# Optimization experiments

Measured on AMD Instinct MI355X. Metric: run time of the kernel, lower is better.

The kernel has to match this reference:

```python
import jax, jax.numpy as jnp
import numpy as np

N = 10000       # num_nodes
E = 160000      # num_edges
F = 128         # num_features
R = 20          # num_rbf_features
L = 3           # num_message_passing_layers
CUT = 3.0       # cutoff_dist
NA = 119        # num_unique_atoms + 1


def _safe_norm(x, axis=-1):
    sq = jnp.sum(x * x, axis=axis)
    return jnp.where(sq > 0, jnp.sqrt(jnp.where(sq > 0, sq, 1.0)), 0.0)


def setup_inputs() -> dict:
    key = jax.random.key(0)
    ks = jax.random.split(key, 20)
    s = 0.05  # weight init scale
    z = jax.random.randint(ks[0], (N,), 1, NA)
    pos = jax.random.uniform(ks[1], (N, 3), dtype=jnp.float32) * 4.0
    idx_i = jax.random.randint(ks[2], (E,), 0, N)
    off = jax.random.randint(ks[3], (E,), 1, N)
    idx_j = (idx_i + off) % N  # no self loops (radius_graph loop=False)
    emb = (jax.random.normal(ks[4], (NA, F), jnp.float32) * s).at[0].set(0.0)
    return {
        'z': z, 'pos': pos, 'idx_i': idx_i, 'idx_j': idx_j, 'emb': emb,
        'msg_w1': jax.random.normal(ks[5], (L, F, F), jnp.float32) * s,
        'msg_b1': jnp.zeros((L, F), jnp.float32),
        'msg_w2': jax.random.normal(ks[6], (L, F, 3 * F), jnp.float32) * s,
        'msg_b2': jnp.zeros((L, 3 * F), jnp.float32),
        'rbf_w': jax.random.normal(ks[7], (L, R, 3 * F), jnp.float32) * s,
        'rbf_b': jnp.zeros((L, 3 * F), jnp.float32),
        'upd_U': jax.random.normal(ks[8], (L, F, F), jnp.float32) * s,
        'upd_V': jax.random.normal(ks[9], (L, F, F), jnp.float32) * s,
        'upd_w1': jax.random.normal(ks[10], (L, 2 * F, F), jnp.float32) * s,
        'upd_b1': jnp.zeros((L, F), jnp.float32),
        'upd_w2': jax.random.normal(ks[11], (L, F, 3 * F), jnp.float32) * s,
        'upd_b2': jnp.zeros((L, 3 * F), jnp.float32),
    }


def reference(z, pos, idx_i, idx_j, emb, msg_w1, msg_b1, msg_w2, msg_b2,
              rbf_w, rbf_b, upd_U, upd_V, upd_w1, upd_b1, upd_w2, upd_b2):
    n_nodes = z.shape[0]
    sfeat = emb[z]                                       # [N, F]
    vfeat = jnp.zeros((n_nodes, F, 3), sfeat.dtype)      # [N, F, 3]

    rel_pos = pos[idx_j] - pos[idx_i]                    # [E, 3]
    rel_dist = jnp.linalg.norm(rel_pos, axis=-1)         # [E]
    rel_dir = rel_pos / rel_dist[:, None]                # [E, 3]
    # cosine cutoff
    cut = 0.5 * (jnp.cos(jnp.pi * rel_dist / CUT) + 1.0) * (rel_dist < CUT)
    # sinusoidal RBF: sin(n*pi*d/cutoff)/d, n = 1..R
    n = jnp.arange(1, R + 1, dtype=sfeat.dtype)
    rbf = jnp.sin(n[None, :] * jnp.pi * rel_dist[:, None] / CUT) / rel_dist[:, None]

    for l in range(L):
        # ---- message block ----
        phi = jax.nn.silu(sfeat @ msg_w1[l] + msg_b1[l]) @ msg_w2[l] + msg_b2[l]  # [N, 3F]
        W = (rbf @ rbf_w[l] + rbf_b[l]) * cut[:, None]                            # [E, 3F]
        phi_W = phi[idx_j] * W                                                    # [E, 3F]
        pw_vv, pw_ss, pw_vs = jnp.split(phi_W, 3, axis=-1)
        sfeat = sfeat + jax.ops.segment_sum(pw_ss, idx_i, num_segments=n_nodes)
        v_edge = vfeat[idx_j] * pw_vv[..., None] + pw_vs[..., None] * rel_dir[:, None, :]
        vfeat = vfeat + jax.ops.segment_sum(v_edge, idx_i, num_segments=n_nodes)

        # ---- update block ----
        Uv = jnp.einsum('nfd,fg->ngd', vfeat, upd_U[l])   # [N, F, 3]
        Vv = jnp.einsum('nfd,fg->ngd', vfeat, upd_V[l])   # [N, F, 3]
        x = jnp.concatenate([_safe_norm(Vv, axis=-1), sfeat], axis=-1)  # [N, 2F]
        a = jax.nn.silu(x @ upd_w1[l] + upd_b1[l]) @ upd_w2[l] + upd_b2[l]  # [N, 3F]
        a_vv, a_sv, a_ss = jnp.split(a, 3, axis=-1)
        vfeat = vfeat + Uv * a_vv[..., None]
        sfeat = sfeat + a_ss + a_sv * jnp.sum(Uv * Vv, axis=-1)

    return sfeat, vfeat
```

## Files before the change

kernel.cpp:

```cpp
#include <hip/hip_runtime.h>
#include <math.h>

#define NN 10000
#define EE 160000
#define FF 128
#define RR 20
#define LL 3
#define CUTOFF 3.0f
#define F3 384
#define PI_F 3.14159265358979323846f


__global__ __launch_bounds__(256) void k_init(const int* __restrict__ z,
                                              const float* __restrict__ emb,
                                              float* __restrict__ sfeat,
                                              float* __restrict__ v,
                                              int* __restrict__ deg) {
    int idx = blockIdx.x * 256 + threadIdx.x;
    if (idx < NN * 3 * FF) v[idx] = 0.f;
    if (idx < NN * FF) {
        int n = idx >> 7, f = idx & 127;
        sfeat[idx] = emb[z[n] * FF + f];
    }
    if (idx < NN) deg[idx] = 0;
}

__global__ __launch_bounds__(256) void k_count(const int* __restrict__ idx_i,
                                               const int* __restrict__ idx_j,
                                               const float* __restrict__ pos,
                                               int* __restrict__ deg) {
    int e = blockIdx.x * 256 + threadIdx.x;
    if (e >= EE) return;
    int i = idx_i[e], j = idx_j[e];
    float dx = pos[j * 3 + 0] - pos[i * 3 + 0];
    float dy = pos[j * 3 + 1] - pos[i * 3 + 1];
    float dz = pos[j * 3 + 2] - pos[i * 3 + 2];
    float sq = dx * dx + dy * dy + dz * dz;
    if (sq < CUTOFF * CUTOFF) atomicAdd(&deg[i], 1);
}

__global__ __launch_bounds__(1024) void k_scan(const int* __restrict__ deg,
                                               int* __restrict__ rowstart,
                                               int* __restrict__ cursor) {
    __shared__ int sd[1024];
    __shared__ int carry;
    if (threadIdx.x == 0) carry = 0;
    __syncthreads();
    for (int base = 0; base < NN; base += 1024) {
        int i = base + (int)threadIdx.x;
        int val = (i < NN) ? deg[i] : 0;
        sd[threadIdx.x] = val;
        __syncthreads();
        for (int off = 1; off < 1024; off <<= 1) {
            int t = (threadIdx.x >= off) ? sd[threadIdx.x - off] : 0;
            __syncthreads();
            sd[threadIdx.x] += t;
            __syncthreads();
        }
        if (i < NN) {
            int ex = carry + sd[threadIdx.x] - val;
            rowstart[i] = ex;
            cursor[i] = ex;
        }
        __syncthreads();
        if (threadIdx.x == 0) carry += sd[1023];
        __syncthreads();
    }
    if (threadIdx.x == 0) rowstart[NN] = carry;
}

__global__ __launch_bounds__(256) void k_fill(const int* __restrict__ idx_i,
                                              const int* __restrict__ idx_j,
                                              const float* __restrict__ pos,
                                              int* __restrict__ cursor,
                                              int* __restrict__ eids) {
    int e = blockIdx.x * 256 + threadIdx.x;
    if (e >= EE) return;
    int i = idx_i[e], j = idx_j[e];
    float dx = pos[j * 3 + 0] - pos[i * 3 + 0];
    float dy = pos[j * 3 + 1] - pos[i * 3 + 1];
    float dz = pos[j * 3 + 2] - pos[i * 3 + 2];
    float sq = dx * dx + dy * dy + dz * dz;
    if (sq < CUTOFF * CUTOFF) {
        int p = atomicAdd(&cursor[i], 1);
        eids[p] = e;
    }
}

__global__ __launch_bounds__(256) void k_permute(const int* __restrict__ idx_i,
                                                 const int* __restrict__ idx_j,
                                                 const float* __restrict__ pos,
                                                 const int* __restrict__ eids,
                                                 const int* __restrict__ rowstart,
                                                 int* __restrict__ j_csr,
                                                 float4* __restrict__ cd_csr,
                                                 float* __restrict__ rbf_csr) {
    int t = blockIdx.x * 256 + threadIdx.x;
    if (t >= rowstart[NN]) return;
    int e = eids[t];
    int i = idx_i[e], j = idx_j[e];
    float dx = pos[j * 3 + 0] - pos[i * 3 + 0];
    float dy = pos[j * 3 + 1] - pos[i * 3 + 1];
    float dz = pos[j * 3 + 2] - pos[i * 3 + 2];
    float sq = dx * dx + dy * dy + dz * dz;
    float dist = sq > 0.f ? sqrtf(sq) : 0.f;
    float inv = dist > 0.f ? 1.f / dist : 0.f;
    float cut = 0.5f * (cosf(PI_F * dist / CUTOFF) + 1.f);
    j_csr[t] = j;
    cd_csr[t] = make_float4(cut, dx * inv, dy * inv, dz * inv);
    float b = PI_F * dist / CUTOFF;
    float* rp = rbf_csr + (size_t)t * RR;
#pragma unroll
    for (int r = 0; r < RR; r++)
        rp[r] = sinf((float)(r + 1) * b) * inv;
}

template <int KTOT, bool SILU>
__global__ __launch_bounds__(256, 4) void k_mlp(const float* __restrict__ A, int KA,
                                                const float* __restrict__ A2,
                                                const float* __restrict__ W,
                                                const float* __restrict__ bias,
                                                float* __restrict__ C, int M, int NOUT) {
    constexpr int STR = 36;
    __shared__ float As[KTOT * STR];
    const int tid = threadIdx.x;
    const int row0 = blockIdx.x * 32;
    const int K2 = KTOT - KA;
    for (int idx = tid; idx < 32 * KTOT; idx += 256) {
        int r = idx / KTOT, k = idx - r * KTOT;
        int row = row0 + r;
        float val = 0.f;
        if (row < M) val = (k < KA) ? A[(size_t)row * KA + k] : A2[(size_t)row * K2 + (k - KA)];
        As[k * STR + r] = val;
    }
    __syncthreads();
    const int cg = tid & 31;
    const int rg = tid >> 5;
    const int c0 = blockIdx.y * 128 + cg * 4;
    const int r0 = rg * 4;
    float4 acc0, acc1, acc2, acc3;
    {
        float4 b = bias ? *reinterpret_cast<const float4*>(bias + c0)
                        : make_float4(0.f, 0.f, 0.f, 0.f);
        acc0 = b; acc1 = b; acc2 = b; acc3 = b;
    }
    for (int k = 0; k < KTOT; k++) {
        float4 w = *reinterpret_cast<const float4*>(W + (size_t)k * NOUT + c0);
        float4 a = *reinterpret_cast<const float4*>(&As[k * STR + r0]);
        acc0.x += a.x * w.x; acc0.y += a.x * w.y; acc0.z += a.x * w.z; acc0.w += a.x * w.w;
        acc1.x += a.y * w.x; acc1.y += a.y * w.y; acc1.z += a.y * w.z; acc1.w += a.y * w.w;
        acc2.x += a.z * w.x; acc2.y += a.z * w.y; acc2.z += a.z * w.z; acc2.w += a.z * w.w;
        acc3.x += a.w * w.x; acc3.y += a.w * w.y; acc3.z += a.w * w.z; acc3.w += a.w * w.w;
    }
#pragma unroll
    for (int p = 0; p < 4; p++) {
        int row = row0 + r0 + p;
        if (row < M) {
            float4 o = (p == 0) ? acc0 : (p == 1) ? acc1 : (p == 2) ? acc2 : acc3;
            if (SILU) {
                o.x = o.x / (1.f + expf(-o.x)); o.y = o.y / (1.f + expf(-o.y));
                o.z = o.z / (1.f + expf(-o.z)); o.w = o.w / (1.f + expf(-o.w));
            }
            *reinterpret_cast<float4*>(C + (size_t)row * NOUT + c0) = o;
        }
    }
}

__global__ __launch_bounds__(256, 4) void k_uv(const float* __restrict__ A,
                                               const float* __restrict__ WU,
                                               const float* __restrict__ WV,
                                               float* __restrict__ CU,
                                               float* __restrict__ CV, int M) {
    constexpr int STR = 36;
    __shared__ float As[128 * STR];
    const int tid = threadIdx.x;
    const int row0 = blockIdx.x * 32;
    for (int idx = tid; idx < 32 * 128; idx += 256) {
        int r = idx >> 7, k = idx & 127;
        int row = row0 + r;
        As[k * STR + r] = (row < M) ? A[(size_t)row * 128 + k] : 0.f;
    }
    __syncthreads();
    const int cg = tid & 31, rg = tid >> 5;
    const int c0 = cg * 4;
    const int r0 = rg * 4;
    float4 u0 = make_float4(0.f,0.f,0.f,0.f), u1 = u0, u2 = u0, u3 = u0;
    float4 v0 = u0, v1 = u0, v2 = u0, v3 = u0;
    for (int k = 0; k < 128; k++) {
        float4 wu = *reinterpret_cast<const float4*>(WU + k * 128 + c0);
        float4 wv = *reinterpret_cast<const float4*>(WV + k * 128 + c0);
        float4 a = *reinterpret_cast<const float4*>(&As[k * STR + r0]);
        u0.x += a.x * wu.x; u0.y += a.x * wu.y; u0.z += a.x * wu.z; u0.w += a.x * wu.w;
        u1.x += a.y * wu.x; u1.y += a.y * wu.y; u1.z += a.y * wu.z; u1.w += a.y * wu.w;
        u2.x += a.z * wu.x; u2.y += a.z * wu.y; u2.z += a.z * wu.z; u2.w += a.z * wu.w;
        u3.x += a.w * wu.x; u3.y += a.w * wu.y; u3.z += a.w * wu.z; u3.w += a.w * wu.w;
        v0.x += a.x * wv.x; v0.y += a.x * wv.y; v0.z += a.x * wv.z; v0.w += a.x * wv.w;
        v1.x += a.y * wv.x; v1.y += a.y * wv.y; v1.z += a.y * wv.z; v1.w += a.y * wv.w;
        v2.x += a.z * wv.x; v2.y += a.z * wv.y; v2.z += a.z * wv.z; v2.w += a.z * wv.w;
        v3.x += a.w * wv.x; v3.y += a.w * wv.y; v3.z += a.w * wv.z; v3.w += a.w * wv.w;
    }
#pragma unroll
    for (int p = 0; p < 4; p++) {
        int row = row0 + r0 + p;
        if (row < M) {
            float4 ou = (p == 0) ? u0 : (p == 1) ? u1 : (p == 2) ? u2 : u3;
            float4 ov = (p == 0) ? v0 : (p == 1) ? v1 : (p == 2) ? v2 : v3;
            *reinterpret_cast<float4*>(CU + (size_t)row * 128 + c0) = ou;
            *reinterpret_cast<float4*>(CV + (size_t)row * 128 + c0) = ov;
        }
    }
}

__global__ __launch_bounds__(256) void k_edge_node(const int* __restrict__ rowstart,
                                                   const int* __restrict__ j_csr,
                                                   const float4* __restrict__ cd_csr,
                                                   const float* __restrict__ rbf_csr,
                                                   const float* __restrict__ phi,
                                                   const float* __restrict__ vold,
                                                   const float* __restrict__ rbf_w,
                                                   const float* __restrict__ rbf_b,
                                                   float* __restrict__ sfeat,
                                                   float* __restrict__ vnew) {
    const int hf = blockIdx.y;
    __shared__ float sW[(RR + 1) * 192];
    for (int idx = threadIdx.x; idx < (RR + 1) * 192; idx += 256) {
        int rr = idx / 192, lc = idx - rr * 192;
        int gc = (lc >> 6) * 128 + hf * 64 + (lc & 63);
        sW[idx] = (rr < RR) ? rbf_w[rr * F3 + gc] : rbf_b[gc];
    }
    __syncthreads();
    const int wave = threadIdx.x >> 6, lane = threadIdx.x & 63;
    const int n = blockIdx.x * 4 + wave;
    const int fb = hf * 64 + lane;
    const float bvv = sW[RR * 192 + lane];
    const float bss = sW[RR * 192 + 64 + lane];
    const float bvs = sW[RR * 192 + 128 + lane];
    float as = 0.f, ad0 = 0.f, ad1 = 0.f, ad2 = 0.f;
    int t = rowstart[n];
    const int t1 = rowstart[n + 1];
    for (; t + 1 < t1; t += 2) {
        const int j0 = j_csr[t], j1 = j_csr[t + 1];
        const float4 cA = cd_csr[t], cB = cd_csr[t + 1];
        const float* rp0 = rbf_csr + (size_t)t * RR;
        float avv0 = bvv, ass0 = bss, avs0 = bvs;
        float avv1 = bvv, ass1 = bss, avs1 = bvs;
#pragma unroll
        for (int q = 0; q < 5; q++) {
            const float4 r0 = *reinterpret_cast<const float4*>(rp0 + q * 4);
            const float4 r1 = *reinterpret_cast<const float4*>(rp0 + RR + q * 4);
            {
                const float wvv = sW[(4*q+0)*192 + lane], wss = sW[(4*q+0)*192 + 64 + lane], wvs = sW[(4*q+0)*192 + 128 + lane];
                avv0 += r0.x * wvv; ass0 += r0.x * wss; avs0 += r0.x * wvs;
                avv1 += r1.x * wvv; ass1 += r1.x * wss; avs1 += r1.x * wvs;
            }
            {
                const float wvv = sW[(4*q+1)*192 + lane], wss = sW[(4*q+1)*192 + 64 + lane], wvs = sW[(4*q+1)*192 + 128 + lane];
                avv0 += r0.y * wvv; ass0 += r0.y * wss; avs0 += r0.y * wvs;
                avv1 += r1.y * wvv; ass1 += r1.y * wss; avs1 += r1.y * wvs;
            }
            {
                const float wvv = sW[(4*q+2)*192 + lane], wss = sW[(4*q+2)*192 + 64 + lane], wvs = sW[(4*q+2)*192 + 128 + lane];
                avv0 += r0.z * wvv; ass0 += r0.z * wss; avs0 += r0.z * wvs;
                avv1 += r1.z * wvv; ass1 += r1.z * wss; avs1 += r1.z * wvs;
            }
            {
                const float wvv = sW[(4*q+3)*192 + lane], wss = sW[(4*q+3)*192 + 64 + lane], wvs = sW[(4*q+3)*192 + 128 + lane];
                avv0 += r0.w * wvv; ass0 += r0.w * wss; avs0 += r0.w * wvs;
                avv1 += r1.w * wvv; ass1 += r1.w * wss; avs1 += r1.w * wvs;
            }
        }
        const size_t p0 = (size_t)j0 * F3 + fb;
        const size_t p1 = (size_t)j1 * F3 + fb;
        const float pvv0 = phi[p0]       * (avv0 * cA.x);
        const float pss0 = phi[p0 + 128] * (ass0 * cA.x);
        const float pvs0 = phi[p0 + 256] * (avs0 * cA.x);
        const float pvv1 = phi[p1]       * (avv1 * cB.x);
        const float pss1 = phi[p1 + 128] * (ass1 * cB.x);
        const float pvs1 = phi[p1 + 256] * (avs1 * cB.x);
        as  += pss0 + pss1;
        ad0 += vold[p0]       * pvv0 + pvs0 * cA.y + vold[p1]       * pvv1 + pvs1 * cB.y;
        ad1 += vold[p0 + 128] * pvv0 + pvs0 * cA.z + vold[p1 + 128] * pvv1 + pvs1 * cB.z;
        ad2 += vold[p0 + 256] * pvv0 + pvs0 * cA.w + vold[p1 + 256] * pvv1 + pvs1 * cB.w;
    }
    if (t < t1) {
        const int j0 = j_csr[t];
        const float4 cA = cd_csr[t];
        const float* rp0 = rbf_csr + (size_t)t * RR;
        float avv0 = bvv, ass0 = bss, avs0 = bvs;
#pragma unroll
        for (int q = 0; q < 5; q++) {
            const float4 r0 = *reinterpret_cast<const float4*>(rp0 + q * 4);
            avv0 += r0.x * sW[(4*q+0)*192 + lane] + r0.y * sW[(4*q+1)*192 + lane]
                  + r0.z * sW[(4*q+2)*192 + lane] + r0.w * sW[(4*q+3)*192 + lane];
            ass0 += r0.x * sW[(4*q+0)*192 + 64 + lane] + r0.y * sW[(4*q+1)*192 + 64 + lane]
                  + r0.z * sW[(4*q+2)*192 + 64 + lane] + r0.w * sW[(4*q+3)*192 + 64 + lane];
            avs0 += r0.x * sW[(4*q+0)*192 + 128 + lane] + r0.y * sW[(4*q+1)*192 + 128 + lane]
                  + r0.z * sW[(4*q+2)*192 + 128 + lane] + r0.w * sW[(4*q+3)*192 + 128 + lane];
        }
        const size_t p0 = (size_t)j0 * F3 + fb;
        const float pvv0 = phi[p0]       * (avv0 * cA.x);
        const float pss0 = phi[p0 + 128] * (ass0 * cA.x);
        const float pvs0 = phi[p0 + 256] * (avs0 * cA.x);
        as  += pss0;
        ad0 += vold[p0]       * pvv0 + pvs0 * cA.y;
        ad1 += vold[p0 + 128] * pvv0 + pvs0 * cA.z;
        ad2 += vold[p0 + 256] * pvv0 + pvs0 * cA.w;
    }
    sfeat[n * FF + fb] += as;
    const size_t vb0 = (size_t)n * F3 + fb;
    vnew[vb0]       = vold[vb0]       + ad0;
    vnew[vb0 + 128] = vold[vb0 + 128] + ad1;
    vnew[vb0 + 256] = vold[vb0 + 256] + ad2;
}

__global__ __launch_bounds__(256) void k_normdot(const float* __restrict__ Uv,
                                                 const float* __restrict__ Vv,
                                                 float* __restrict__ vnorm,
                                                 float* __restrict__ dotb) {
    int idx = blockIdx.x * 256 + threadIdx.x;
    if (idx >= NN * FF) return;
    int n = idx >> 7, g = idx & 127;
    const float* uv = Uv + (size_t)n * F3 + g;
    const float* vv = Vv + (size_t)n * F3 + g;
    float u0 = uv[0], u1 = uv[FF], u2 = uv[2 * FF];
    float w0 = vv[0], w1 = vv[FF], w2 = vv[2 * FF];
    float sq = w0 * w0 + w1 * w1 + w2 * w2;
    vnorm[idx] = sq > 0.f ? sqrtf(sq) : 0.f;
    dotb[idx] = u0 * w0 + u1 * w1 + u2 * w2;
}

__global__ __launch_bounds__(256) void k_update(const float* __restrict__ a,
                                                const float* __restrict__ Uv,
                                                const float* __restrict__ dotb,
                                                float* __restrict__ v,
                                                float* __restrict__ sfeat) {
    int idx = blockIdx.x * 256 + threadIdx.x;
    if (idx >= NN * FF) return;
    int n = idx >> 7, g = idx & 127;
    float avv = a[(size_t)n * F3 + g];
    float asv = a[(size_t)n * F3 + 128 + g];
    float ass = a[(size_t)n * F3 + 256 + g];
#pragma unroll
    for (int d = 0; d < 3; d++)
        v[(size_t)n * F3 + d * FF + g] += Uv[(size_t)n * F3 + d * FF + g] * avv;
    sfeat[idx] += ass + asv * dotb[idx];
}

__global__ __launch_bounds__(256) void k_outv(const float* __restrict__ v,
                                              float* __restrict__ outv) {
    int idx = blockIdx.x * 256 + threadIdx.x;
    if (idx >= NN * FF * 3) return;
    int n = idx / F3;
    int rem = idx - n * F3;
    int f = rem / 3;
    int d = rem - f * 3;
    outv[idx] = v[n * F3 + d * FF + f];
}

extern "C" void kernel_launch(void* const* d_in, const int* in_sizes, int n_in,
                              void* d_out, int out_size, void* d_ws, size_t ws_size,
                              hipStream_t stream) {
    const int*   z      = (const int*)d_in[0];
    const float* pos    = (const float*)d_in[1];
    const int*   idx_i  = (const int*)d_in[2];
    const int*   idx_j  = (const int*)d_in[3];
    const float* emb    = (const float*)d_in[4];
    const float* msg_w1 = (const float*)d_in[5];
    const float* msg_b1 = (const float*)d_in[6];
    const float* msg_w2 = (const float*)d_in[7];
    const float* msg_b2 = (const float*)d_in[8];
    const float* rbf_w  = (const float*)d_in[9];
    const float* rbf_b  = (const float*)d_in[10];
    const float* upd_U  = (const float*)d_in[11];
    const float* upd_V  = (const float*)d_in[12];
    const float* upd_w1 = (const float*)d_in[13];
    const float* upd_b1 = (const float*)d_in[14];
    const float* upd_w2 = (const float*)d_in[15];
    const float* upd_b2 = (const float*)d_in[16];

    float* sfeat = (float*)d_out;
    float* outv  = sfeat + NN * FF;

    float* ws    = (float*)d_ws;
    float* va    = ws;
    float* vb    = va + NN * F3;
    float* phi   = vb + NN * F3;
    float* h     = phi + NN * F3;
    float* Uvb   = h + NN * FF;
    float* Vvb   = Uvb + NN * F3;
    float* vnorm = Vvb + NN * F3;
    float* dotb  = vnorm + NN * FF;
    float4* cd_csr = (float4*)(dotb + NN * FF);
    float* rbf_csr = (float*)(cd_csr + EE);
    int*   j_csr     = (int*)(rbf_csr + (size_t)EE * RR);
    int*   deg       = j_csr + EE;
    int*   rowstart  = deg + NN;
    int*   cursor    = rowstart + NN + 1;
    int*   eids      = cursor + NN;

    const dim3 blk(256);
    const dim3 gE((EE + 255) / 256);
    k_init<<<dim3((NN * 3 * FF) / 256), blk, 0, stream>>>(z, emb, sfeat, va, deg);
    k_count<<<gE, blk, 0, stream>>>(idx_i, idx_j, pos, deg);
    k_scan<<<dim3(1), dim3(1024), 0, stream>>>(deg, rowstart, cursor);
    k_fill<<<gE, blk, 0, stream>>>(idx_i, idx_j, pos, cursor, eids);
    k_permute<<<gE, blk, 0, stream>>>(idx_i, idx_j, pos, eids, rowstart,
                                      j_csr, cd_csr, rbf_csr);

    float* vcur = va;
    float* vnxt = vb;
    const int gN32  = (NN + 31) / 32;
    const int g3N32 = (3 * NN + 31) / 32;

    for (int l = 0; l < LL; l++) {
        const float* mw1 = msg_w1 + l * FF * FF;
        const float* mb1 = msg_b1 + l * FF;
        const float* mw2 = msg_w2 + l * FF * F3;
        const float* mb2 = msg_b2 + l * F3;
        const float* rw  = rbf_w + l * RR * F3;
        const float* rb  = rbf_b + l * F3;
        const float* uU  = upd_U + l * FF * FF;
        const float* uV  = upd_V + l * FF * FF;
        const float* uw1 = upd_w1 + l * 2 * FF * FF;
        const float* ub1 = upd_b1 + l * FF;
        const float* uw2 = upd_w2 + l * FF * F3;
        const float* ub2 = upd_b2 + l * F3;

        k_mlp<128, true><<<dim3(gN32, 1), blk, 0, stream>>>(sfeat, 128, nullptr, mw1, mb1, h, NN, 128);
        k_mlp<128, false><<<dim3(gN32, 3), blk, 0, stream>>>(h, 128, nullptr, mw2, mb2, phi, NN, F3);

        k_edge_node<<<dim3(NN / 4, 2), blk, 0, stream>>>(rowstart, j_csr, cd_csr, rbf_csr,
                                                         phi, vcur, rw, rb, sfeat, vnxt);

        k_uv<<<dim3(g3N32), blk, 0, stream>>>(vnxt, uU, uV, Uvb, Vvb, 3 * NN);
        k_normdot<<<dim3((NN * FF) / 256), blk, 0, stream>>>(Uvb, Vvb, vnorm, dotb);

        k_mlp<256, true><<<dim3(gN32, 1), blk, 0, stream>>>(vnorm, 128, sfeat, uw1, ub1, h, NN, 128);
        k_mlp<128, false><<<dim3(gN32, 3), blk, 0, stream>>>(h, 128, nullptr, uw2, ub2, phi, NN, F3);

        k_update<<<dim3((NN * FF) / 256), blk, 0, stream>>>(phi, Uvb, dotb, vnxt, sfeat);

        float* tmp = vcur; vcur = vnxt; vnxt = tmp;
    }

    k_outv<<<dim3((NN * FF * 3 + 255) / 256), blk, 0, stream>>>(vcur, outv);
}
```

Baseline: 1.071 ms.

## Stage weights in LDS for node GEMMs and widen edge kernel to all features

The MLP and U/V GEMM kernels now stage 32-row chunks of the weight matrix in shared memory and read activation rows directly from global memory, with some variants computing 8 rows per thread (64-row tiles). The edge-node kernel now loads the whole RBF weight matrix into LDS and has each wave cover all 128 features of one node, processing 4 edges per iteration. The 2-way feature split is gone, so the CSR/rbf data and weights are no longer fetched twice. This raises register pressure from the 8-row and 4-edge accumulators, and the activation reads from global memory are strided across lanes, which may lower memory efficiency.

```diff
diff --git a/kernel.cpp b/kernel.cpp
--- a/kernel.cpp
+++ b/kernel.cpp
@@ -115,55 +115,78 @@
         rp[r] = sinf((float)(r + 1) * b) * inv;
 }
 
-template <int KTOT, bool SILU>
+template <int KTOT, int ROWS, bool SILU>
 __global__ __launch_bounds__(256, 4) void k_mlp(const float* __restrict__ A, int KA,
                                                 const float* __restrict__ A2,
                                                 const float* __restrict__ W,
                                                 const float* __restrict__ bias,
                                                 float* __restrict__ C, int M, int NOUT) {
-    constexpr int STR = 36;
-    __shared__ float As[KTOT * STR];
+    constexpr int RT = ROWS / 8;
+    __shared__ float Ws[32 * 132];
     const int tid = threadIdx.x;
-    const int row0 = blockIdx.x * 32;
-    const int K2 = KTOT - KA;
-    for (int idx = tid; idx < 32 * KTOT; idx += 256) {
-        int r = idx / KTOT, k = idx - r * KTOT;
-        int row = row0 + r;
-        float val = 0.f;
-        if (row < M) val = (k < KA) ? A[(size_t)row * KA + k] : A2[(size_t)row * K2 + (k - KA)];
-        As[k * STR + r] = val;
-    }
-    __syncthreads();
-    const int cg = tid & 31;
-    const int rg = tid >> 5;
-    const int c0 = blockIdx.y * 128 + cg * 4;
-    const int r0 = rg * 4;
-    float4 acc0, acc1, acc2, acc3;
+    const int cg = tid & 31, rg = tid >> 5;
+    const int cbase = blockIdx.y * 128;
+    const int c0 = cbase + cg * 4;
+    const int r0 = blockIdx.x * ROWS + rg * RT;
+    float4 acc0, acc1, acc2, acc3, acc4, acc5, acc6, acc7;
     {
         float4 b = bias ? *reinterpret_cast<const float4*>(bias + c0)
                         : make_float4(0.f, 0.f, 0.f, 0.f);
         acc0 = b; acc1 = b; acc2 = b; acc3 = b;
-    }
-    for (int k = 0; k < KTOT; k++) {
-        float4 w = *reinterpret_cast<const float4*>(W + (size_t)k * NOUT + c0);
-        float4 a = *reinterpret_cast<const float4*>(&As[k * STR + r0]);
-        acc0.x += a.x * w.x; acc0.y += a.x * w.y; acc0.z += a.x * w.z; acc0.w += a.x * w.w;
-        acc1.x += a.y * w.x; acc1.y += a.y * w.y; acc1.z += a.y * w.z; acc1.w += a.y * w.w;
-        acc2.x += a.z * w.x; acc2.y += a.z * w.y; acc2.z += a.z * w.z; acc2.w += a.z * w.w;
-        acc3.x += a.w * w.x; acc3.y += a.w * w.y; acc3.z += a.w * w.z; acc3.w += a.w * w.w;
-    }
-#pragma unroll
-    for (int p = 0; p < 4; p++) {
-        int row = row0 + r0 + p;
-        if (row < M) {
-            float4 o = (p == 0) ? acc0 : (p == 1) ? acc1 : (p == 2) ? acc2 : acc3;
-            if (SILU) {
-                o.x = o.x / (1.f + expf(-o.x)); o.y = o.y / (1.f + expf(-o.y));
-                o.z = o.z / (1.f + expf(-o.z)); o.w = o.w / (1.f + expf(-o.w));
+        acc4 = b; acc5 = b; acc6 = b; acc7 = b;
+    }
+    const int K2 = KTOT - KA;
+    for (int kc = 0; kc < KTOT; kc += 32) {
+        __syncthreads();
+        for (int idx = tid; idx < 32 * 128; idx += 256) {
+            int kk = idx >> 7, c = idx & 127;
+            Ws[kk * 132 + c] = W[(size_t)(kc + kk) * NOUT + cbase + c];
+        }
+        __syncthreads();
+        const float* Ab; int ks, koff;
+        if (kc < KA) { Ab = A; ks = KA; koff = 0; }
+        else         { Ab = A2; ks = K2; koff = KA; }
+        const float* a0 = Ab + (size_t)min(r0 + 0, M - 1) * ks + (kc - koff);
+        const float* a1 = Ab + (size_t)min(r0 + 1, M - 1) * ks + (kc - koff);
+        const float* a2 = Ab + (size_t)min(r0 + 2, M - 1) * ks + (kc - koff);
+        const float* a3 = Ab + (size_t)min(r0 + 3, M - 1) * ks + (kc - koff);
+        const float* a4 = a0; const float* a5 = a0;
+        const float* a6 = a0; const float* a7 = a0;
+        if constexpr (RT == 8) {
+            a4 = Ab + (size_t)min(r0 + 4, M - 1) * ks + (kc - koff);
+            a5 = Ab + (size_t)min(r0 + 5, M - 1) * ks + (kc - koff);
+            a6 = Ab + (size_t)min(r0 + 6, M - 1) * ks + (kc - koff);
+            a7 = Ab + (size_t)min(r0 + 7, M - 1) * ks + (kc - koff);
+        }
+#pragma unroll 4
+        for (int kk = 0; kk < 32; kk++) {
+            float4 w = *reinterpret_cast<const float4*>(&Ws[kk * 132 + cg * 4]);
+            float v0 = a0[kk], v1 = a1[kk], v2 = a2[kk], v3 = a3[kk];
+            acc0.x += v0 * w.x; acc0.y += v0 * w.y; acc0.z += v0 * w.z; acc0.w += v0 * w.w;
+            acc1.x += v1 * w.x; acc1.y += v1 * w.y; acc1.z += v1 * w.z; acc1.w += v1 * w.w;
+            acc2.x += v2 * w.x; acc2.y += v2 * w.y; acc2.z += v2 * w.z; acc2.w += v2 * w.w;
+            acc3.x += v3 * w.x; acc3.y += v3 * w.y; acc3.z += v3 * w.z; acc3.w += v3 * w.w;
+            if constexpr (RT == 8) {
+                float v4 = a4[kk], v5 = a5[kk], v6 = a6[kk], v7 = a7[kk];
+                acc4.x += v4 * w.x; acc4.y += v4 * w.y; acc4.z += v4 * w.z; acc4.w += v4 * w.w;
+                acc5.x += v5 * w.x; acc5.y += v5 * w.y; acc5.z += v5 * w.z; acc5.w += v5 * w.w;
+                acc6.x += v6 * w.x; acc6.y += v6 * w.y; acc6.z += v6 * w.z; acc6.w += v6 * w.w;
+                acc7.x += v7 * w.x; acc7.y += v7 * w.y; acc7.z += v7 * w.z; acc7.w += v7 * w.w;
             }
-            *reinterpret_cast<float4*>(C + (size_t)row * NOUT + c0) = o;
-        }
-    }
+        }
+    }
+#define STORE_ROW(P, ACC)                                                  \
+    if (P < RT && r0 + P < M) {                                            \
+        float4 o = ACC;                                                    \
+        if constexpr (SILU) {                                              \
+            o.x = o.x / (1.f + expf(-o.x)); o.y = o.y / (1.f + expf(-o.y));\
+            o.z = o.z / (1.f + expf(-o.z)); o.w = o.w / (1.f + expf(-o.w));\
+        }                                                                  \
+        *reinterpret_cast<float4*>(C + (size_t)(r0 + P) * NOUT + c0) = o;  \
+    }
+    STORE_ROW(0, acc0) STORE_ROW(1, acc1) STORE_ROW(2, acc2) STORE_ROW(3, acc3)
+    STORE_ROW(4, acc4) STORE_ROW(5, acc5) STORE_ROW(6, acc6) STORE_ROW(7, acc7)
+#undef STORE_ROW
 }
 
 __global__ __launch_bounds__(256, 4) void k_uv(const float* __restrict__ A,
@@ -171,146 +194,170 @@
                                                const float* __restrict__ WV,
                                                float* __restrict__ CU,
                                                float* __restrict__ CV, int M) {
-    constexpr int STR = 36;
-    __shared__ float As[128 * STR];
+    __shared__ float WUs[32 * 132];
+    __shared__ float WVs[32 * 132];
     const int tid = threadIdx.x;
-    const int row0 = blockIdx.x * 32;
-    for (int idx = tid; idx < 32 * 128; idx += 256) {
-        int r = idx >> 7, k = idx & 127;
-        int row = row0 + r;
-        As[k * STR + r] = (row < M) ? A[(size_t)row * 128 + k] : 0.f;
-    }
-    __syncthreads();
     const int cg = tid & 31, rg = tid >> 5;
     const int c0 = cg * 4;
-    const int r0 = rg * 4;
-    float4 u0 = make_float4(0.f,0.f,0.f,0.f), u1 = u0, u2 = u0, u3 = u0;
-    float4 v0 = u0, v1 = u0, v2 = u0, v3 = u0;
-    for (int k = 0; k < 128; k++) {
-        float4 wu = *reinterpret_cast<const float4*>(WU + k * 128 + c0);
-        float4 wv = *reinterpret_cast<const float4*>(WV + k * 128 + c0);
-        float4 a = *reinterpret_cast<const float4*>(&As[k * STR + r0]);
-        u0.x += a.x * wu.x; u0.y += a.x * wu.y; u0.z += a.x * wu.z; u0.w += a.x * wu.w;
-        u1.x += a.y * wu.x; u1.y += a.y * wu.y; u1.z += a.y * wu.z; u1.w += a.y * wu.w;
-        u2.x += a.z * wu.x; u2.y += a.z * wu.y; u2.z += a.z * wu.z; u2.w += a.z * wu.w;
-        u3.x += a.w * wu.x; u3.y += a.w * wu.y; u3.z += a.w * wu.z; u3.w += a.w * wu.w;
-        v0.x += a.x * wv.x; v0.y += a.x * wv.y; v0.z += a.x * wv.z; v0.w += a.x * wv.w;
-        v1.x += a.y * wv.x; v1.y += a.y * wv.y; v1.z += a.y * wv.z; v1.w += a.y * wv.w;
-        v2.x += a.z * wv.x; v2.y += a.z * wv.y; v2.z += a.z * wv.z; v2.w += a.z * wv.w;
-        v3.x += a.w * wv.x; v3.y += a.w * wv.y; v3.z += a.w * wv.z; v3.w += a.w * wv.w;
-    }
-#pragma unroll
-    for (int p = 0; p < 4; p++) {
-        int row = row0 + r0 + p;
-        if (row < M) {
-            float4 ou = (p == 0) ? u0 : (p == 1) ? u1 : (p == 2) ? u2 : u3;
-            float4 ov = (p == 0) ? v0 : (p == 1) ? v1 : (p == 2) ? v2 : v3;
-            *reinterpret_cast<float4*>(CU + (size_t)row * 128 + c0) = ou;
-            *reinterpret_cast<float4*>(CV + (size_t)row * 128 + c0) = ov;
-        }
-    }
-}
-
-__global__ __launch_bounds__(256) void k_edge_node(const int* __restrict__ rowstart,
-                                                   const int* __restrict__ j_csr,
-                                                   const float4* __restrict__ cd_csr,
-                                                   const float* __restrict__ rbf_csr,
-                                                   const float* __restrict__ phi,
-                                                   const float* __restrict__ vold,
-                                                   const float* __restrict__ rbf_w,
-                                                   const float* __restrict__ rbf_b,
-                                                   float* __restrict__ sfeat,
-                                                   float* __restrict__ vnew) {
-    const int hf = blockIdx.y;
-    __shared__ float sW[(RR + 1) * 192];
-    for (int idx = threadIdx.x; idx < (RR + 1) * 192; idx += 256) {
-        int rr = idx / 192, lc = idx - rr * 192;
-        int gc = (lc >> 6) * 128 + hf * 64 + (lc & 63);
-        sW[idx] = (rr < RR) ? rbf_w[rr * F3 + gc] : rbf_b[gc];
-    }
+    const int r0 = blockIdx.x * 64 + rg * 8;
+    float4 u0, u1, u2, u3, u4, u5, u6, u7;
+    float4 q0, q1, q2, q3, q4, q5, q6, q7;
+    {
+        float4 zz = make_float4(0.f, 0.f, 0.f, 0.f);
+        u0 = zz; u1 = zz; u2 = zz; u3 = zz; u4 = zz; u5 = zz; u6 = zz; u7 = zz;
+        q0 = zz; q1 = zz; q2 = zz; q3 = zz; q4 = zz; q5 = zz; q6 = zz; q7 = zz;
+    }
+    for (int kc = 0; kc < 128; kc += 32) {
+        __syncthreads();
+        for (int idx = tid; idx < 32 * 128; idx += 256) {
+            int kk = idx >> 7, c = idx & 127;
+            WUs[kk * 132 + c] = WU[(size_t)(kc + kk) * 128 + c];
+            WVs[kk * 132 + c] = WV[(size_t)(kc + kk) * 128 + c];
+        }
+        __syncthreads();
+        const float* a0 = A + (size_t)min(r0 + 0, M - 1) * 128 + kc;
+        const float* a1 = A + (size_t)min(r0 + 1, M - 1) * 128 + kc;
+        const float* a2 = A + (size_t)min(r0 + 2, M - 1) * 128 + kc;
+        const float* a3 = A + (size_t)min(r0 + 3, M - 1) * 128 + kc;
+        const float* a4 = A + (size_t)min(r0 + 4, M - 1) * 128 + kc;
+        const float* a5 = A + (size_t)min(r0 + 5, M - 1) * 128 + kc;
+        const float* a6 = A + (size_t)min(r0 + 6, M - 1) * 128 + kc;
+        const float* a7 = A + (size_t)min(r0 + 7, M - 1) * 128 + kc;
+#pragma unroll 4
+        for (int kk = 0; kk < 32; kk++) {
+            float4 wu = *reinterpret_cast<const float4*>(&WUs[kk * 132 + c0]);
+            float4 wv = *reinterpret_cast<const float4*>(&WVs[kk * 132 + c0]);
+            float v0 = a0[kk], v1 = a1[kk], v2 = a2[kk], v3 = a3[kk];
+            float v4 = a4[kk], v5 = a5[kk], v6 = a6[kk], v7 = a7[kk];
+            u0.x += v0 * wu.x; u0.y += v0 * wu.y; u0.z += v0 * wu.z; u0.w += v0 * wu.w;
+            u1.x += v1 * wu.x; u1.y += v1 * wu.y; u1.z += v1 * wu.z; u1.w += v1 * wu.w;
+            u2.x += v2 * wu.x; u2.y += v2 * wu.y; u2.z += v2 * wu.z; u2.w += v2 * wu.w;
+            u3.x += v3 * wu.x; u3.y += v3 * wu.y; u3.z += v3 * wu.z; u3.w += v3 * wu.w;
+            u4.x += v4 * wu.x; u4.y += v4 * wu.y; u4.z += v4 * wu.z; u4.w += v4 * wu.w;
+            u5.x += v5 * wu.x; u5.y += v5 * wu.y; u5.z += v5 * wu.z; u5.w += v5 * wu.w;
+            u6.x += v6 * wu.x; u6.y += v6 * wu.y; u6.z += v6 * wu.z; u6.w += v6 * wu.w;
+            u7.x += v7 * wu.x; u7.y += v7 * wu.y; u7.z += v7 * wu.z; u7.w += v7 * wu.w;
+            q0.x += v0 * wv.x; q0.y += v0 * wv.y; q0.z += v0 * wv.z; q0.w += v0 * wv.w;
+            q1.x += v1 * wv.x; q1.y += v1 * wv.y; q1.z += v1 * wv.z; q1.w += v1 * wv.w;
+            q2.x += v2 * wv.x; q2.y += v2 * wv.y; q2.z += v2 * wv.z; q2.w += v2 * wv.w;
+            q3.x += v3 * wv.x; q3.y += v3 * wv.y; q3.z += v3 * wv.z; q3.w += v3 * wv.w;
+            q4.x += v4 * wv.x; q4.y += v4 * wv.y; q4.z += v4 * wv.z; q4.w += v4 * wv.w;
+            q5.x += v5 * wv.x; q5.y += v5 * wv.y; q5.z += v5 * wv.z; q5.w += v5 * wv.w;
+            q6.x += v6 * wv.x; q6.y += v6 * wv.y; q6.z += v6 * wv.z; q6.w += v6 * wv.w;
+            q7.x += v7 * wv.x; q7.y += v7 * wv.y; q7.z += v7 * wv.z; q7.w += v7 * wv.w;
+        }
+    }
+#define STORE_UV(P, UA, QA)                                                    \
+    if (r0 + P < M) {                                                         \
+        *reinterpret_cast<float4*>(CU + (size_t)(r0 + P) * 128 + c0) = UA;    \
+        *reinterpret_cast<float4*>(CV + (size_t)(r0 + P) * 128 + c0) = QA;    \
+    }
+    STORE_UV(0, u0, q0) STORE_UV(1, u1, q1) STORE_UV(2, u2, q2) STORE_UV(3, u3, q3)
+    STORE_UV(4, u4, q4) STORE_UV(5, u5, q5) STORE_UV(6, u6, q6) STORE_UV(7, u7, q7)
+#undef STORE_UV
+}
+
+#define CSTEP(RA, RB, RC, RD, ROW)                                            \
+    {                                                                         \
+        const float* swr = &sW[(ROW) * F3 + lane];                            \
+        float wv;                                                             \
+        wv = swr[0];   w0.x += (RA)*wv; w0.y += (RB)*wv; w0.z += (RC)*wv; w0.w += (RD)*wv; \
+        wv = swr[64];  w1.x += (RA)*wv; w1.y += (RB)*wv; w1.z += (RC)*wv; w1.w += (RD)*wv; \
+        wv = swr[128]; w2.x += (RA)*wv; w2.y += (RB)*wv; w2.z += (RC)*wv; w2.w += (RD)*wv; \
+        wv = swr[192]; w3.x += (RA)*wv; w3.y += (RB)*wv; w3.z += (RC)*wv; w3.w += (RD)*wv; \
+        wv = swr[256]; w4.x += (RA)*wv; w4.y += (RB)*wv; w4.z += (RC)*wv; w4.w += (RD)*wv; \
+        wv = swr[320]; w5.x += (RA)*wv; w5.y += (RB)*wv; w5.z += (RC)*wv; w5.w += (RD)*wv; \
+    }
+
+#define EDGE_EPI(WSEL, JV, CD)                                                \
+    {                                                                         \
+        const size_t pb = (size_t)(JV) * F3 + lane;                           \
+        const float cc = (CD).x;                                              \
+        const float pw0 = phi[pb]       * (w0.WSEL * cc);                     \
+        const float pw1 = phi[pb + 64]  * (w1.WSEL * cc);                     \
+        const float pw2 = phi[pb + 128] * (w2.WSEL * cc);                     \
+        const float pw3 = phi[pb + 192] * (w3.WSEL * cc);                     \
+        const float pw4 = phi[pb + 256] * (w4.WSEL * cc);                     \
+        const float pw5 = phi[pb + 320] * (w5.WSEL * cc);                     \
+        as0 += pw2; as1 += pw3;                                               \
+        ad00 += vold[pb]       * pw0 + pw4 * (CD).y;                          \
+        ad01 += vold[pb + 64]  * pw1 + pw5 * (CD).y;                          \
+        ad10 += vold[pb + 128] * pw0 + pw4 * (CD).z;                          \
+        ad11 += vold[pb + 192] * pw1 + pw5 * (CD).z;                          \
+        ad20 += vold[pb + 256] * pw0 + pw4 * (CD).w;                          \
+        ad21 += vold[pb + 320] * pw1 + pw5 * (CD).w;                          \
+    }
+
+__global__ __launch_bounds__(512, 4) void k_edge_node(const int* __restrict__ rowstart,
+                                                      const int* __restrict__ j_csr,
+                                                      const float4* __restrict__ cd_csr,
+                                                      const float* __restrict__ rbf_csr,
+                                                      const float* __restrict__ phi,
+                                                      const float* __restrict__ vold,
+                                                      const float* __restrict__ rbf_w,
+                                                      const float* __restrict__ rbf_b,
+                                                      float* __restrict__ sfeat,
+                                                      float* __restrict__ vnew) {
+    __shared__ float sW[RR * F3 + F3];
+    for (int idx = threadIdx.x; idx < RR * F3; idx += 512) sW[idx] = rbf_w[idx];
+    for (int idx = threadIdx.x; idx < F3; idx += 512) sW[RR * F3 + idx] = rbf_b[idx];
     __syncthreads();
     const int wave = threadIdx.x >> 6, lane = threadIdx.x & 63;
-    const int n = blockIdx.x * 4 + wave;
-    const int fb = hf * 64 + lane;
-    const float bvv = sW[RR * 192 + lane];
-    const float bss = sW[RR * 192 + 64 + lane];
-    const float bvs = sW[RR * 192 + 128 + lane];
-    float as = 0.f, ad0 = 0.f, ad1 = 0.f, ad2 = 0.f;
-    int t = rowstart[n];
+    const int n = blockIdx.x * 8 + wave;
+    float as0 = 0.f, as1 = 0.f;
+    float ad00 = 0.f, ad01 = 0.f, ad10 = 0.f, ad11 = 0.f, ad20 = 0.f, ad21 = 0.f;
+    const float bb0 = sW[RR * F3 + lane];
+    const float bb1 = sW[RR * F3 + 64 + lane];
+    const float bb2 = sW[RR * F3 + 128 + lane];
+    const float bb3 = sW[RR * F3 + 192 + lane];
+    const float bb4 = sW[RR * F3 + 256 + lane];
+    const float bb5 = sW[RR * F3 + 320 + lane];
     const int t1 = rowstart[n + 1];
-    for (; t + 1 < t1; t += 2) {
-        const int j0 = j_csr[t], j1 = j_csr[t + 1];
-        const float4 cA = cd_csr[t], cB = cd_csr[t + 1];
-        const float* rp0 = rbf_csr + (size_t)t * RR;
-        float avv0 = bvv, ass0 = bss, avs0 = bvs;
-        float avv1 = bvv, ass1 = bss, avs1 = bvs;
+    for (int t = rowstart[n]; t < t1; t += 4) {
+        const int i0 = t;
+        const int i1 = (t + 1 < t1) ? t + 1 : t;
+        const int i2 = (t + 2 < t1) ? t + 2 : t;
+        const int i3 = (t + 3 < t1) ? t + 3 : t;
+        const int j0 = j_csr[i0], j1 = j_csr[i1], j2 = j_csr[i2], j3 = j_csr[i3];
+        const float4 cd0 = cd_csr[i0];
+        const float4 cd1 = (t + 1 < t1) ? cd_csr[i1] : make_float4(0.f, 0.f, 0.f, 0.f);
+        const float4 cd2 = (t + 2 < t1) ? cd_csr[i2] : make_float4(0.f, 0.f, 0.f, 0.f);
+        const float4 cd3 = (t + 3 < t1) ? cd_csr[i3] : make_float4(0.f, 0.f, 0.f, 0.f);
+        const float* rp0 = rbf_csr + (size_t)i0 * RR;
+        const float* rp1 = rbf_csr + (size_t)i1 * RR;
+        const float* rp2 = rbf_csr + (size_t)i2 * RR;
+        const float* rp3 = rbf_csr + (size_t)i3 * RR;
+        float4 w0 = make_float4(bb0, bb0, bb0, bb0);
+        float4 w1 = make_float4(bb1, bb1, bb1, bb1);
+        float4 w2 = make_float4(bb2, bb2, bb2, bb2);
+        float4 w3 = make_float4(bb3, bb3, bb3, bb3);
+        float4 w4 = make_float4(bb4, bb4, bb4, bb4);
+        float4 w5 = make_float4(bb5, bb5, bb5, bb5);
 #pragma unroll
         for (int q = 0; q < 5; q++) {
-            const float4 r0 = *reinterpret_cast<const float4*>(rp0 + q * 4);
-            const float4 r1 = *reinterpret_cast<const float4*>(rp0 + RR + q * 4);
-            {
-                const float wvv = sW[(4*q+0)*192 + lane], wss = sW[(4*q+0)*192 + 64 + lane], wvs = sW[(4*q+0)*192 + 128 + lane];
-                avv0 += r0.x * wvv; ass0 += r0.x * wss; avs0 += r0.x * wvs;
-                avv1 += r1.x * wvv; ass1 += r1.x * wss; avs1 += r1.x * wvs;
-            }
-            {
-                const float wvv = sW[(4*q+1)*192 + lane], wss = sW[(4*q+1)*192 + 64 + lane], wvs = sW[(4*q+1)*192 + 128 + lane];
-                avv0 += r0.y * wvv; ass0 += r0.y * wss; avs0 += r0.y * wvs;
-                avv1 += r1.y * wvv; ass1 += r1.y * wss; avs1 += r1.y * wvs;
-            }
-            {
-                const float wvv = sW[(4*q+2)*192 + lane], wss = sW[(4*q+2)*192 + 64 + lane], wvs = sW[(4*q+2)*192 + 128 + lane];
-                avv0 += r0.z * wvv; ass0 += r0.z * wss; avs0 += r0.z * wvs;
-                avv1 += r1.z * wvv; ass1 += r1.z * wss; avs1 += r1.z * wvs;
-            }
-            {
-                const float wvv = sW[(4*q+3)*192 + lane], wss = sW[(4*q+3)*192 + 64 + lane], wvs = sW[(4*q+3)*192 + 128 + lane];
-                avv0 += r0.w * wvv; ass0 += r0.w * wss; avs0 += r0.w * wvs;
-                avv1 += r1.w * wvv; ass1 += r1.w * wss; avs1 += r1.w * wvs;
-            }
-        }
-        const size_t p0 = (size_t)j0 * F3 + fb;
-        const size_t p1 = (size_t)j1 * F3 + fb;
-        const float pvv0 = phi[p0]       * (avv0 * cA.x);
-        const float pss0 = phi[p0 + 128] * (ass0 * cA.x);
-        const float pvs0 = phi[p0 + 256] * (avs0 * cA.x);
-        const float pvv1 = phi[p1]       * (avv1 * cB.x);
-        const float pss1 = phi[p1 + 128] * (ass1 * cB.x);
-        const float pvs1 = phi[p1 + 256] * (avs1 * cB.x);
-        as  += pss0 + pss1;
-        ad0 += vold[p0]       * pvv0 + pvs0 * cA.y + vold[p1]       * pvv1 + pvs1 * cB.y;
-        ad1 += vold[p0 + 128] * pvv0 + pvs0 * cA.z + vold[p1 + 128] * pvv1 + pvs1 * cB.z;
-        ad2 += vold[p0 + 256] * pvv0 + pvs0 * cA.w + vold[p1 + 256] * pvv1 + pvs1 * cB.w;
-    }
-    if (t < t1) {
-        const int j0 = j_csr[t];
-        const float4 cA = cd_csr[t];
-        const float* rp0 = rbf_csr + (size_t)t * RR;
-        float avv0 = bvv, ass0 = bss, avs0 = bvs;
-#pragma unroll
-        for (int q = 0; q < 5; q++) {
-            const float4 r0 = *reinterpret_cast<const float4*>(rp0 + q * 4);
-            avv0 += r0.x * sW[(4*q+0)*192 + lane] + r0.y * sW[(4*q+1)*192 + lane]
-                  + r0.z * sW[(4*q+2)*192 + lane] + r0.w * sW[(4*q+3)*192 + lane];
-            ass0 += r0.x * sW[(4*q+0)*192 + 64 + lane] + r0.y * sW[(4*q+1)*192 + 64 + lane]
-                  + r0.z * sW[(4*q+2)*192 + 64 + lane] + r0.w * sW[(4*q+3)*192 + 64 + lane];
-            avs0 += r0.x * sW[(4*q+0)*192 + 128 + lane] + r0.y * sW[(4*q+1)*192 + 128 + lane]
-                  + r0.z * sW[(4*q+2)*192 + 128 + lane] + r0.w * sW[(4*q+3)*192 + 128 + lane];
-        }
-        const size_t p0 = (size_t)j0 * F3 + fb;
-        const float pvv0 = phi[p0]       * (avv0 * cA.x);
-        const float pss0 = phi[p0 + 128] * (ass0 * cA.x);
-        const float pvs0 = phi[p0 + 256] * (avs0 * cA.x);
-        as  += pss0;
-        ad0 += vold[p0]       * pvv0 + pvs0 * cA.y;
-        ad1 += vold[p0 + 128] * pvv0 + pvs0 * cA.z;
-        ad2 += vold[p0 + 256] * pvv0 + pvs0 * cA.w;
-    }
-    sfeat[n * FF + fb] += as;
-    const size_t vb0 = (size_t)n * F3 + fb;
-    vnew[vb0]       = vold[vb0]       + ad0;
-    vnew[vb0 + 128] = vold[vb0 + 128] + ad1;
-    vnew[vb0 + 256] = vold[vb0 + 256] + ad2;
+            const float4 ra = *reinterpret_cast<const float4*>(rp0 + q * 4);
+            const float4 rb = *reinterpret_cast<const float4*>(rp1 + q * 4);
+            const float4 rc = *reinterpret_cast<const float4*>(rp2 + q * 4);
+            const float4 rd = *reinterpret_cast<const float4*>(rp3 + q * 4);
+            CSTEP(ra.x, rb.x, rc.x, rd.x, 4 * q + 0)
+            CSTEP(ra.y, rb.y, rc.y, rd.y, 4 * q + 1)
+            CSTEP(ra.z, rb.z, rc.z, rd.z, 4 * q + 2)
+            CSTEP(ra.w, rb.w, rc.w, rd.w, 4 * q + 3)
+        }
+        EDGE_EPI(x, j0, cd0)
+        EDGE_EPI(y, j1, cd1)
+        EDGE_EPI(z, j2, cd2)
+        EDGE_EPI(w, j3, cd3)
+    }
+    sfeat[n * FF + lane]      += as0;
+    sfeat[n * FF + 64 + lane] += as1;
+    const size_t vb0 = (size_t)n * F3 + lane;
+    vnew[vb0]       = vold[vb0]       + ad00;
+    vnew[vb0 + 64]  = vold[vb0 + 64]  + ad01;
+    vnew[vb0 + 128] = vold[vb0 + 128] + ad10;
+    vnew[vb0 + 192] = vold[vb0 + 192] + ad11;
+    vnew[vb0 + 256] = vold[vb0 + 256] + ad20;
+    vnew[vb0 + 320] = vold[vb0 + 320] + ad21;
 }
 
 __global__ __launch_bounds__(256) void k_normdot(const float* __restrict__ Uv,
@@ -410,7 +457,8 @@
     float* vcur = va;
     float* vnxt = vb;
     const int gN32  = (NN + 31) / 32;
-    const int g3N32 = (3 * NN + 31) / 32;
+    const int gN64  = (NN + 63) / 64;
+    const int g3N64 = (3 * NN + 63) / 64;
 
     for (int l = 0; l < LL; l++) {
         const float* mw1 = msg_w1 + l * FF * FF;
@@ -426,17 +474,17 @@
         const float* uw2 = upd_w2 + l * FF * F3;
         const float* ub2 = upd_b2 + l * F3;
 
-        k_mlp<128, true><<<dim3(gN32, 1), blk, 0, stream>>>(sfeat, 128, nullptr, mw1, mb1, h, NN, 128);
-        k_mlp<128, false><<<dim3(gN32, 3), blk, 0, stream>>>(h, 128, nullptr, mw2, mb2, phi, NN, F3);
-
-        k_edge_node<<<dim3(NN / 4, 2), blk, 0, stream>>>(rowstart, j_csr, cd_csr, rbf_csr,
-                                                         phi, vcur, rw, rb, sfeat, vnxt);
-
-        k_uv<<<dim3(g3N32), blk, 0, stream>>>(vnxt, uU, uV, Uvb, Vvb, 3 * NN);
+        k_mlp<128, 32, true><<<dim3(gN32, 1), blk, 0, stream>>>(sfeat, 128, nullptr, mw1, mb1, h, NN, 128);
+        k_mlp<128, 64, false><<<dim3(gN64, 3), blk, 0, stream>>>(h, 128, nullptr, mw2, mb2, phi, NN, F3);
+
+        k_edge_node<<<dim3(NN / 8), dim3(512), 0, stream>>>(rowstart, j_csr, cd_csr, rbf_csr,
+                                                            phi, vcur, rw, rb, sfeat, vnxt);
+
+        k_uv<<<dim3(g3N64), blk, 0, stream>>>(vnxt, uU, uV, Uvb, Vvb, 3 * NN);
         k_normdot<<<dim3((NN * FF) / 256), blk, 0, stream>>>(Uvb, Vvb, vnorm, dotb);
 
-        k_mlp<256, true><<<dim3(gN32, 1), blk, 0, stream>>>(vnorm, 128, sfeat, uw1, ub1, h, NN, 128);
-        k_mlp<128, false><<<dim3(gN32, 3), blk, 0, stream>>>(h, 128, nullptr, uw2, ub2, phi, NN, F3);
+        k_mlp<256, 32, true><<<dim3(gN32, 1), blk, 0, stream>>>(vnorm, 128, sfeat, uw1, ub1, h, NN, 128);
+        k_mlp<128, 64, false><<<dim3(gN64, 3), blk, 0, stream>>>(h, 128, nullptr, uw2, ub2, phi, NN, F3);
 
         k_update<<<dim3((NN * FF) / 256), blk, 0, stream>>>(phi, Uvb, dotb, vnxt, sfeat);
 
```

Measured after the change: 2.739 ms. +155.6%, slower.
